# Performance work log

Hardware: AMD Instinct MI355X
Metric: run time of the kernel (lower is better)

## Reference

```python
import jax, jax.numpy as jnp
import numpy as np

N_NODES = 100000
N_EDGES = 1600000
IN_C, HID_C, OUT_C = 165, 256, 2


def setup_inputs() -> dict:
    key = jax.random.key(0)
    ks = jax.random.split(key, 7)
    x = jax.random.normal(ks[0], (N_NODES, IN_C), dtype=jnp.float32)
    edge_index = jax.random.randint(ks[1], (2, N_EDGES), 0, N_NODES, dtype=jnp.int64)
    # Glorot-ish scaled weights
    W1_l = jax.random.normal(ks[2], (IN_C, HID_C), dtype=jnp.float32) / np.sqrt(IN_C)
    W1_r = jax.random.normal(ks[3], (IN_C, HID_C), dtype=jnp.float32) / np.sqrt(IN_C)
    W2_l = jax.random.normal(ks[4], (HID_C, OUT_C), dtype=jnp.float32) / np.sqrt(HID_C)
    W2_r = jax.random.normal(ks[5], (HID_C, OUT_C), dtype=jnp.float32) / np.sqrt(HID_C)
    b1 = jnp.zeros((HID_C,), dtype=jnp.float32)
    b2 = jnp.zeros((OUT_C,), dtype=jnp.float32)
    return {"x": x, "edge_index": edge_index, "W1_l": W1_l, "b1": b1,
            "W1_r": W1_r, "W2_l": W2_l, "b2": b2, "W2_r": W2_r}


def _sage_conv(h, src, dst, n_nodes, Wl, b, Wr):
    # mean aggregation of neighbor messages (src -> dst), as in PyG SAGEConv
    agg = jax.ops.segment_sum(h[src], dst, num_segments=n_nodes)  # [N, C]
    deg = jax.ops.segment_sum(jnp.ones_like(dst, dtype=h.dtype), dst,
                              num_segments=n_nodes)               # [N]
    mean = agg / jnp.maximum(deg, 1.0)[:, None]
    # out = lin_l(aggr) + lin_r(root); bias lives on lin_l
    return mean @ Wl + b + h @ Wr


def reference(x, edge_index, W1_l, b1, W1_r, W2_l, b2, W2_r):
    src, dst = edge_index[0], edge_index[1]
    n = x.shape[0]
    h = jax.nn.relu(_sage_conv(x, src, dst, n, W1_l, b1, W1_r))
    out = _sage_conv(h, src, dst, n, W2_l, b2, W2_r)
    return out
```

## Files before the change

kernel.cpp:

```cpp
#include <hip/hip_runtime.h>

#define N_NODES 100000
#define N_EDGES 1600000
#define IN_C 165
#define HID_C 256
#define OUT_C 2

#define XPAD 168
#define LDSROW 360
#define NBLK_SCAN 98

typedef short bf16x8 __attribute__((ext_vector_type(8)));
typedef float f32x4 __attribute__((ext_vector_type(4)));

__device__ inline unsigned short f2bf(float f) {
    unsigned int u = __float_as_uint(f);
    u += 0x7fffu + ((u >> 16) & 1u);
    return (unsigned short)(u >> 16);
}
__device__ inline float bf2f(unsigned short h) {
    return __uint_as_float(((unsigned int)h) << 16);
}
__device__ inline unsigned int pack2bf(float a, float b) {
    return (unsigned int)f2bf(a) | ((unsigned int)f2bf(b) << 16);
}


__launch_bounds__(1024)
__global__ void k_scan1(const int* __restrict__ deg, int* __restrict__ incl,
                        int* __restrict__ btot) {
    const int tid = threadIdx.x;
    const int idx = blockIdx.x * 1024 + tid;
    const int lane = tid & 63, wid = tid >> 6;
    __shared__ int ws[16];
    int v = (idx < N_NODES) ? deg[idx] : 0;
    int s = v;
#pragma unroll
    for (int off = 1; off < 64; off <<= 1) {
        int t = __shfl_up(s, off);
        if (lane >= off) s += t;
    }
    if (lane == 63) ws[wid] = s;
    __syncthreads();
    if (wid == 0) {
        int p = (lane < 16) ? ws[lane] : 0;
#pragma unroll
        for (int off = 1; off < 16; off <<= 1) {
            int t = __shfl_up(p, off);
            if (lane >= off) p += t;
        }
        if (lane < 16) ws[lane] = p;
    }
    __syncthreads();
    int blockincl = s + (wid > 0 ? ws[wid - 1] : 0);
    if (idx < N_NODES) incl[idx] = blockincl;
    if (tid == 1023) btot[blockIdx.x] = blockincl;
}

__global__ void k_scan2(int* __restrict__ btot) {
    const int lane = threadIdx.x;
    int a = (2 * lane < NBLK_SCAN) ? btot[2 * lane] : 0;
    int b = (2 * lane + 1 < NBLK_SCAN) ? btot[2 * lane + 1] : 0;
    int p = a + b;
#pragma unroll
    for (int off = 1; off < 64; off <<= 1) {
        int t = __shfl_up(p, off);
        if (lane >= off) p += t;
    }
    if (2 * lane < NBLK_SCAN) btot[2 * lane] = p - b;
    if (2 * lane + 1 < NBLK_SCAN) btot[2 * lane + 1] = p;
}

__launch_bounds__(1024)
__global__ void k_scan3(const int* __restrict__ deg, int* incl_cursor,
                        const int* __restrict__ btot, int* __restrict__ rowptr) {
    const int idx = blockIdx.x * 1024 + threadIdx.x;
    if (idx == 0) rowptr[0] = 0;
    if (idx >= N_NODES) return;
    int off = (blockIdx.x > 0) ? btot[blockIdx.x - 1] : 0;
    int v = incl_cursor[idx] + off;
    rowptr[idx + 1] = v;
    incl_cursor[idx] = v - deg[idx];
}

#define FILL_GRID 2048
__global__ void k_fill(const int* __restrict__ src, const int* __restrict__ dst,
                       int* __restrict__ cursor, int* __restrict__ csr) {
    const int role = blockIdx.x & 7;
    const int nchunk = gridDim.x >> 3;
    const int lo = role * (N_NODES / 8);
    const int hi = lo + (N_NODES / 8);
    for (int e = (blockIdx.x >> 3) * 256 + threadIdx.x; e < N_EDGES;
         e += nchunk * 256) {
        int d = dst[e];
        int s = src[e];
        if (d >= lo && d < hi) {
            int pos = atomicAdd(&cursor[d], 1);
            csr[pos] = s;
        }
    }
}

__global__ void k_cvt(const float* __restrict__ x, const int* __restrict__ dst,
                      uint2* __restrict__ xb2, int* __restrict__ deg) {
    int idx = blockIdx.x * blockDim.x + threadIdx.x;
    if (idx < N_EDGES) atomicAdd(&deg[dst[idx]], 1);
    if (idx >= N_NODES * 42) return;
    int n = idx / 42;
    int t = idx - n * 42;
    int c = 4 * t;
    float f0 = x[(size_t)n * IN_C + c];
    float f1 = (c + 1 < IN_C) ? x[(size_t)n * IN_C + c + 1] : 0.f;
    float f2 = (c + 2 < IN_C) ? x[(size_t)n * IN_C + c + 2] : 0.f;
    float f3 = (c + 3 < IN_C) ? x[(size_t)n * IN_C + c + 3] : 0.f;
    uint2 p;
    p.x = pack2bf(f0, f1);
    p.y = pack2bf(f2, f3);
    xb2[idx] = p;
}

__global__ void k_wt(const float* __restrict__ W1l, const float* __restrict__ W1r,
                     unsigned short* __restrict__ Wt) {
    int k = blockIdx.x;
    int c = threadIdx.x;
    float v = 0.0f;
    if (k < IN_C) v = W1l[k * HID_C + c];
    else if (k >= XPAD && k < XPAD + IN_C) v = W1r[(k - XPAD) * HID_C + c];
    Wt[(size_t)c * 352 + k] = f2bf(v);
}

__global__ void k_agg1b(const int* __restrict__ rowptr, const int* __restrict__ csr,
                        const uint2* __restrict__ xb2, uint2* __restrict__ aggb2) {
    int n = (blockIdx.x * blockDim.x + threadIdx.x) >> 6;
    if (n >= N_NODES) return;
    const int lane = threadIdx.x & 63;
    const bool act = lane < 42;
    int beg = rowptr[n], end = rowptr[n + 1];
    float a0 = 0.f, a1 = 0.f, a2 = 0.f, a3 = 0.f;
    int j = beg;
#define ACC(u) { a0 += bf2f((unsigned short)((u).x & 0xffffu)); \
                 a1 += bf2f((unsigned short)((u).x >> 16)); \
                 a2 += bf2f((unsigned short)((u).y & 0xffffu)); \
                 a3 += bf2f((unsigned short)((u).y >> 16)); }
    for (; j + 7 < end; j += 8) {
        uint2 u[8];
#pragma unroll
        for (int q = 0; q < 8; ++q) {
            int s = csr[j + q];
            u[q] = act ? xb2[(size_t)s * 42 + lane] : make_uint2(0, 0);
        }
#pragma unroll
        for (int q = 0; q < 8; ++q) ACC(u[q]);
    }
    for (; j + 3 < end; j += 4) {
        uint2 u[4];
#pragma unroll
        for (int q = 0; q < 4; ++q) {
            int s = csr[j + q];
            u[q] = act ? xb2[(size_t)s * 42 + lane] : make_uint2(0, 0);
        }
#pragma unroll
        for (int q = 0; q < 4; ++q) ACC(u[q]);
    }
    for (; j < end; ++j) {
        int s0 = csr[j];
        uint2 u0 = act ? xb2[(size_t)s0 * 42 + lane] : make_uint2(0, 0);
        ACC(u0);
    }
#undef ACC
    if (act) {
        float invd = 1.0f / fmaxf((float)(end - beg), 1.0f);
        uint2 p;
        p.x = pack2bf(a0 * invd, a1 * invd);
        p.y = pack2bf(a2 * invd, a3 * invd);
        aggb2[(size_t)n * 42 + lane] = p;
    }
}

__launch_bounds__(256)
__global__ void k_gemm1(const unsigned short* __restrict__ aggb,
                        const unsigned short* __restrict__ xb,
                        const unsigned short* __restrict__ Wt,
                        const float* __restrict__ b1,
                        const float* __restrict__ W2l, const float* __restrict__ W2r,
                        float* __restrict__ yz) {
    __shared__ __align__(16) unsigned short lds[64 * LDSROW];
    const int tid = threadIdx.x;
    const int lane = tid & 63;
    const int w = tid >> 6;
    const int node0 = blockIdx.x * 64;

#pragma unroll
    for (int it = 0; it < 12; ++it) {
        int idx = tid + it * 256;
        if (idx < 64 * 45) {
            int row = idx / 45;
            int c = idx - row * 45;
            int n = node0 + row;
            uint4 v = make_uint4(0, 0, 0, 0);
            if (n < N_NODES) {
                if (c < 21)      v = *(const uint4*)&aggb[(size_t)n * XPAD + c * 8];
                else if (c < 42) v = *(const uint4*)&xb[(size_t)n * XPAD + (c - 21) * 8];
            }
            *(uint4*)&lds[row * LDSROW + c * 8] = v;
        }
    }
    __syncthreads();

    const int arow = lane & 15;
    const int kgrp = lane >> 4;
    const int colbase = w * 64;
    f32x4 acc[4][4] = {};

    for (int ks = 0; ks < 11; ++ks) {
        const int k0 = ks * 32 + kgrp * 8;
        bf16x8 bfr[4], afr[4];
#pragma unroll
        for (int n = 0; n < 4; ++n)
            bfr[n] = *(const bf16x8*)&Wt[(size_t)(colbase + n * 16 + arow) * 352 + k0];
#pragma unroll
        for (int m = 0; m < 4; ++m)
            afr[m] = *(const bf16x8*)&lds[(m * 16 + arow) * LDSROW + k0];
#pragma unroll
        for (int m = 0; m < 4; ++m)
#pragma unroll
            for (int n = 0; n < 4; ++n)
                acc[m][n] = __builtin_amdgcn_mfma_f32_16x16x32_bf16(afr[m], bfr[n],
                                                                    acc[m][n], 0, 0, 0);
    }

    float b1c[4];
    float2 wl[4], wr[4];
#pragma unroll
    for (int n = 0; n < 4; ++n) {
        int c = colbase + n * 16 + arow;
        b1c[n] = b1[c];
        wl[n] = *(const float2*)&W2l[c * 2];
        wr[n] = *(const float2*)&W2r[c * 2];
    }
    __syncthreads();
    float* part = (float*)lds;

#pragma unroll
    for (int m = 0; m < 4; ++m)
#pragma unroll
        for (int r = 0; r < 4; ++r) {
            float y0 = 0.f, y1 = 0.f, z0 = 0.f, z1 = 0.f;
#pragma unroll
            for (int n = 0; n < 4; ++n) {
                float h = fmaxf(acc[m][n][r] + b1c[n], 0.0f);
                y0 = fmaf(h, wl[n].x, y0); y1 = fmaf(h, wl[n].y, y1);
                z0 = fmaf(h, wr[n].x, z0); z1 = fmaf(h, wr[n].y, z1);
            }
#pragma unroll
            for (int off = 1; off < 16; off <<= 1) {
                y0 += __shfl_xor(y0, off); y1 += __shfl_xor(y1, off);
                z0 += __shfl_xor(z0, off); z1 += __shfl_xor(z1, off);
            }
            if (arow == 0) {
                int row = m * 16 + kgrp * 4 + r;
                float* p = &part[(w * 64 + row) * 4];
                p[0] = y0; p[1] = y1; p[2] = z0; p[3] = z1;
            }
        }
    __syncthreads();

    {
        int row = tid >> 2;
        int ch = tid & 3;
        float s = part[row * 4 + ch] + part[(256 + row * 4) + ch] +
                  part[(512 + row * 4) + ch] + part[(768 + row * 4) + ch];
        int node = node0 + row;
        if (node < N_NODES) yz[(size_t)node * 4 + ch] = s;
    }
}

__global__ void k_layer2(const int* __restrict__ rowptr, const int* __restrict__ csr,
                         const float* __restrict__ yz, const float* __restrict__ b2,
                         float* __restrict__ out) {
    int n = (blockIdx.x * blockDim.x + threadIdx.x) >> 6;
    if (n >= N_NODES) return;
    const int lane = threadIdx.x & 63;
    int beg = rowptr[n], end = rowptr[n + 1];
    float y0 = 0.f, y1 = 0.f;
    for (int i = beg + lane; i < end; i += 64) {
        int s = csr[i];
        float2 v = *(const float2*)&yz[(size_t)s * 4];
        y0 += v.x; y1 += v.y;
    }
#pragma unroll
    for (int off = 32; off >= 1; off >>= 1) {
        y0 += __shfl_xor(y0, off);
        y1 += __shfl_xor(y1, off);
    }
    if (lane == 0) {
        float invd = 1.0f / fmaxf((float)(end - beg), 1.0f);
        float2 o;
        o.x = y0 * invd + b2[0] + yz[(size_t)n * 4 + 2];
        o.y = y1 * invd + b2[1] + yz[(size_t)n * 4 + 3];
        *(float2*)&out[n * 2] = o;
    }
}

extern "C" void kernel_launch(void* const* d_in, const int* in_sizes, int n_in,
                              void* d_out, int out_size, void* d_ws, size_t ws_size,
                              hipStream_t stream) {
    const float* x   = (const float*)d_in[0];
    const int*   ei  = (const int*)d_in[1];
    const int*   src = ei;
    const int*   dst = ei + N_EDGES;
    const float* W1l = (const float*)d_in[2];
    const float* b1  = (const float*)d_in[3];
    const float* W1r = (const float*)d_in[4];
    const float* W2l = (const float*)d_in[5];
    const float* b2  = (const float*)d_in[6];
    const float* W2r = (const float*)d_in[7];
    float* out = (float*)d_out;

    int* wsi = (int*)d_ws;
    int* csr    = wsi;
    int* rowptr = wsi + 1600000;
    unsigned short* xb   = (unsigned short*)(wsi + 1700004);
    unsigned short* aggb = xb + (size_t)N_NODES * XPAD;
    unsigned short* Wt   = aggb + (size_t)N_NODES * XPAD;
    float* yz            = (float*)(Wt + 256 * 352);
    int* deg    = (int*)yz;
    int* inccur = (int*)yz + N_NODES;
    int* btot   = (int*)yz + 2 * N_NODES;

    hipMemsetAsync(deg, 0, N_NODES * sizeof(int), stream);

    k_cvt<<<(N_NODES * 42 + 255) / 256, 256, 0, stream>>>(x, dst, (uint2*)xb, deg);
    k_wt<<<352, 256, 0, stream>>>(W1l, W1r, Wt);
    k_scan1<<<NBLK_SCAN, 1024, 0, stream>>>(deg, inccur, btot);
    k_scan2<<<1, 64, 0, stream>>>(btot);
    k_scan3<<<NBLK_SCAN, 1024, 0, stream>>>(deg, inccur, btot, rowptr);
    k_fill<<<FILL_GRID, 256, 0, stream>>>(src, dst, inccur, csr);
    k_agg1b<<<(N_NODES * 64 + 255) / 256, 256, 0, stream>>>(rowptr, csr,
                                                            (const uint2*)xb,
                                                            (uint2*)aggb);
    k_gemm1<<<(N_NODES + 63) / 64, 256, 0, stream>>>(aggb, xb, Wt, b1, W2l, W2r, yz);
    k_layer2<<<(N_NODES * 64 + 255) / 256, 256, 0, stream>>>(rowptr, csr, yz, b2, out);
}
```

Baseline: 466.3 us.

## Split degree counting into partitioned kernel and halve gemm1 node tile

Moves the degree atomics out of the conversion kernel into a separate k_deg kernel. It partitions destination ranges across block roles, the same way the fill kernel does, to improve atomic locality. The src load in k_fill now happens only for edges that pass the range filter. k_gemm1 now processes 32 nodes per block instead of 64, which doubles the grid and lowers LDS and register use per block. The cost is more reloads of the weight tile and one extra kernel launch.

```diff
diff --git a/kernel.cpp b/kernel.cpp
--- a/kernel.cpp
+++ b/kernel.cpp
@@ -9,6 +9,7 @@
 #define XPAD 168
 #define LDSROW 360
 #define NBLK_SCAN 98
+#define GNT 32
 
 typedef short bf16x8 __attribute__((ext_vector_type(8)));
 typedef float f32x4 __attribute__((ext_vector_type(4)));
@@ -25,6 +26,18 @@
     return (unsigned int)f2bf(a) | ((unsigned int)f2bf(b) << 16);
 }
 
+
+__global__ void k_deg(const int* __restrict__ dst, int* __restrict__ deg) {
+    const int role = blockIdx.x & 7;
+    const int nchunk = gridDim.x >> 3;
+    const int lo = role * (N_NODES / 8);
+    const int hi = lo + (N_NODES / 8);
+    for (int e = (blockIdx.x >> 3) * 256 + threadIdx.x; e < N_EDGES;
+         e += nchunk * 256) {
+        int d = dst[e];
+        if (d >= lo && d < hi) atomicAdd(&deg[d], 1);
+    }
+}
 
 __launch_bounds__(1024)
 __global__ void k_scan1(const int* __restrict__ deg, int* __restrict__ incl,
@@ -93,18 +106,16 @@
     for (int e = (blockIdx.x >> 3) * 256 + threadIdx.x; e < N_EDGES;
          e += nchunk * 256) {
         int d = dst[e];
-        int s = src[e];
         if (d >= lo && d < hi) {
+            int s = src[e];
             int pos = atomicAdd(&cursor[d], 1);
             csr[pos] = s;
         }
     }
 }
 
-__global__ void k_cvt(const float* __restrict__ x, const int* __restrict__ dst,
-                      uint2* __restrict__ xb2, int* __restrict__ deg) {
+__global__ void k_cvt(const float* __restrict__ x, uint2* __restrict__ xb2) {
     int idx = blockIdx.x * blockDim.x + threadIdx.x;
-    if (idx < N_EDGES) atomicAdd(&deg[dst[idx]], 1);
     if (idx >= N_NODES * 42) return;
     int n = idx / 42;
     int t = idx - n * 42;
@@ -184,45 +195,41 @@
                         const float* __restrict__ b1,
                         const float* __restrict__ W2l, const float* __restrict__ W2r,
                         float* __restrict__ yz) {
-    __shared__ __align__(16) unsigned short lds[64 * LDSROW];
+    __shared__ __align__(16) unsigned short lds[GNT * LDSROW];
     const int tid = threadIdx.x;
     const int lane = tid & 63;
     const int w = tid >> 6;
-    const int node0 = blockIdx.x * 64;
-
-#pragma unroll
-    for (int it = 0; it < 12; ++it) {
-        int idx = tid + it * 256;
-        if (idx < 64 * 45) {
-            int row = idx / 45;
-            int c = idx - row * 45;
-            int n = node0 + row;
-            uint4 v = make_uint4(0, 0, 0, 0);
-            if (n < N_NODES) {
-                if (c < 21)      v = *(const uint4*)&aggb[(size_t)n * XPAD + c * 8];
-                else if (c < 42) v = *(const uint4*)&xb[(size_t)n * XPAD + (c - 21) * 8];
-            }
-            *(uint4*)&lds[row * LDSROW + c * 8] = v;
-        }
+    const int node0 = blockIdx.x * GNT;
+
+    for (int idx = tid; idx < GNT * 45; idx += 256) {
+        int row = idx / 45;
+        int c = idx - row * 45;
+        int n = node0 + row;
+        uint4 v = make_uint4(0, 0, 0, 0);
+        if (n < N_NODES) {
+            if (c < 21)      v = *(const uint4*)&aggb[(size_t)n * XPAD + c * 8];
+            else if (c < 42) v = *(const uint4*)&xb[(size_t)n * XPAD + (c - 21) * 8];
+        }
+        *(uint4*)&lds[row * LDSROW + c * 8] = v;
     }
     __syncthreads();
 
     const int arow = lane & 15;
     const int kgrp = lane >> 4;
     const int colbase = w * 64;
-    f32x4 acc[4][4] = {};
+    f32x4 acc[2][4] = {};
 
     for (int ks = 0; ks < 11; ++ks) {
         const int k0 = ks * 32 + kgrp * 8;
-        bf16x8 bfr[4], afr[4];
+        bf16x8 bfr[4], afr[2];
 #pragma unroll
         for (int n = 0; n < 4; ++n)
             bfr[n] = *(const bf16x8*)&Wt[(size_t)(colbase + n * 16 + arow) * 352 + k0];
 #pragma unroll
-        for (int m = 0; m < 4; ++m)
+        for (int m = 0; m < 2; ++m)
             afr[m] = *(const bf16x8*)&lds[(m * 16 + arow) * LDSROW + k0];
 #pragma unroll
-        for (int m = 0; m < 4; ++m)
+        for (int m = 0; m < 2; ++m)
 #pragma unroll
             for (int n = 0; n < 4; ++n)
                 acc[m][n] = __builtin_amdgcn_mfma_f32_16x16x32_bf16(afr[m], bfr[n],
@@ -242,7 +249,7 @@
     float* part = (float*)lds;
 
 #pragma unroll
-    for (int m = 0; m < 4; ++m)
+    for (int m = 0; m < 2; ++m)
 #pragma unroll
         for (int r = 0; r < 4; ++r) {
             float y0 = 0.f, y1 = 0.f, z0 = 0.f, z1 = 0.f;
@@ -259,17 +266,17 @@
             }
             if (arow == 0) {
                 int row = m * 16 + kgrp * 4 + r;
-                float* p = &part[(w * 64 + row) * 4];
+                float* p = &part[(w * GNT + row) * 4];
                 p[0] = y0; p[1] = y1; p[2] = z0; p[3] = z1;
             }
         }
     __syncthreads();
 
-    {
+    if (tid < GNT * 4) {
         int row = tid >> 2;
         int ch = tid & 3;
-        float s = part[row * 4 + ch] + part[(256 + row * 4) + ch] +
-                  part[(512 + row * 4) + ch] + part[(768 + row * 4) + ch];
+        float s = part[row * 4 + ch] + part[(GNT * 4 + row * 4) + ch] +
+                  part[(GNT * 8 + row * 4) + ch] + part[(GNT * 12 + row * 4) + ch];
         int node = node0 + row;
         if (node < N_NODES) yz[(size_t)node * 4 + ch] = s;
     }
@@ -330,8 +337,9 @@
 
     hipMemsetAsync(deg, 0, N_NODES * sizeof(int), stream);
 
-    k_cvt<<<(N_NODES * 42 + 255) / 256, 256, 0, stream>>>(x, dst, (uint2*)xb, deg);
+    k_cvt<<<(N_NODES * 42 + 255) / 256, 256, 0, stream>>>(x, (uint2*)xb);
     k_wt<<<352, 256, 0, stream>>>(W1l, W1r, Wt);
+    k_deg<<<FILL_GRID, 256, 0, stream>>>(dst, deg);
     k_scan1<<<NBLK_SCAN, 1024, 0, stream>>>(deg, inccur, btot);
     k_scan2<<<1, 64, 0, stream>>>(btot);
     k_scan3<<<NBLK_SCAN, 1024, 0, stream>>>(deg, inccur, btot, rowptr);
@@ -339,6 +347,7 @@
     k_agg1b<<<(N_NODES * 64 + 255) / 256, 256, 0, stream>>>(rowptr, csr,
                                                             (const uint2*)xb,
                                                             (uint2*)aggb);
-    k_gemm1<<<(N_NODES + 63) / 64, 256, 0, stream>>>(aggb, xb, Wt, b1, W2l, W2r, yz);
+    k_gemm1<<<(N_NODES + GNT - 1) / GNT, 256, 0, stream>>>(aggb, xb, Wt, b1,
+                                                           W2l, W2r, yz);
     k_layer2<<<(N_NODES * 64 + 255) / 256, 256, 0, stream>>>(rowptr, csr, yz, b2, out);
 }
```

Result: no change. 474.7 us (+1.8%).

## Pre-bucket edges by destination range before CSR fill

Applied to the files above, without the earlier changes.

Adds a k_bucket pass that counts degrees and scatters (src,dst) pairs into eight per-role staging buckets, each a contiguous dst range, using a workspace region later overwritten by aggregation. The fill kernel then reads only its own bucket instead of every role block scanning all edges and discarding seven eighths of them. This cuts redundant edge reads in the fill from about eight passes to one, at the cost of an extra kernel that writes and rereads 8-byte pairs. Degree counting moves from the conversion kernel into the bucket kernel.

```diff
diff --git a/kernel.cpp b/kernel.cpp
--- a/kernel.cpp
+++ b/kernel.cpp
@@ -9,6 +9,8 @@
 #define XPAD 168
 #define LDSROW 360
 #define NBLK_SCAN 98
+#define ROLE_N (N_NODES / 8)
+#define STAGE_CAP 208000
 
 typedef short bf16x8 __attribute__((ext_vector_type(8)));
 typedef float f32x4 __attribute__((ext_vector_type(4)));
@@ -83,28 +85,61 @@
     incl_cursor[idx] = v - deg[idx];
 }
 
+#define BUCKET_EPB 2048
+__launch_bounds__(256)
+__global__ void k_bucket(const int* __restrict__ src, const int* __restrict__ dst,
+                         int* __restrict__ deg, int* __restrict__ rolecnt,
+                         int2* __restrict__ stage) {
+    __shared__ int lcnt[8];
+    __shared__ int lbase[8];
+    const int tid = threadIdx.x;
+    if (tid < 8) lcnt[tid] = 0;
+    __syncthreads();
+    const int e0 = blockIdx.x * BUCKET_EPB;
+    int sv[8], dv[8], rv[8], lr[8];
+#pragma unroll
+    for (int i = 0; i < 8; ++i) {
+        int e = e0 + tid + i * 256;
+        if (e < N_EDGES) {
+            dv[i] = dst[e];
+            sv[i] = src[e];
+            rv[i] = dv[i] / ROLE_N;
+            atomicAdd(&deg[dv[i]], 1);
+            lr[i] = atomicAdd(&lcnt[rv[i]], 1);
+        }
+    }
+    __syncthreads();
+    if (tid < 8) lbase[tid] = atomicAdd(&rolecnt[tid], lcnt[tid]);
+    __syncthreads();
+#pragma unroll
+    for (int i = 0; i < 8; ++i) {
+        int e = e0 + tid + i * 256;
+        if (e < N_EDGES) {
+            int r = rv[i];
+            stage[(size_t)r * STAGE_CAP + lbase[r] + lr[i]] =
+                make_int2(sv[i], dv[i]);
+        }
+    }
+}
+
 #define FILL_GRID 2048
-__global__ void k_fill(const int* __restrict__ src, const int* __restrict__ dst,
-                       int* __restrict__ cursor, int* __restrict__ csr) {
+__global__ void k_fill2(const int2* __restrict__ stage,
+                        const int* __restrict__ rolecnt,
+                        int* __restrict__ cursor, int* __restrict__ csr) {
     const int role = blockIdx.x & 7;
     const int nchunk = gridDim.x >> 3;
-    const int lo = role * (N_NODES / 8);
-    const int hi = lo + (N_NODES / 8);
-    for (int e = (blockIdx.x >> 3) * 256 + threadIdx.x; e < N_EDGES;
-         e += nchunk * 256) {
-        int d = dst[e];
-        int s = src[e];
-        if (d >= lo && d < hi) {
-            int pos = atomicAdd(&cursor[d], 1);
-            csr[pos] = s;
-        }
-    }
-}
-
-__global__ void k_cvt(const float* __restrict__ x, const int* __restrict__ dst,
-                      uint2* __restrict__ xb2, int* __restrict__ deg) {
+    const int cnt = rolecnt[role];
+    const int2* s = stage + (size_t)role * STAGE_CAP;
+    for (int i = (blockIdx.x >> 3) * 256 + threadIdx.x; i < cnt;
+         i += nchunk * 256) {
+        int2 p = s[i];
+        int pos = atomicAdd(&cursor[p.y], 1);
+        csr[pos] = p.x;
+    }
+}
+
+__global__ void k_cvt(const float* __restrict__ x, uint2* __restrict__ xb2) {
     int idx = blockIdx.x * blockDim.x + threadIdx.x;
-    if (idx < N_EDGES) atomicAdd(&deg[dst[idx]], 1);
     if (idx >= N_NODES * 42) return;
     int n = idx / 42;
     int t = idx - n * 42;
@@ -324,18 +359,22 @@
     unsigned short* aggb = xb + (size_t)N_NODES * XPAD;
     unsigned short* Wt   = aggb + (size_t)N_NODES * XPAD;
     float* yz            = (float*)(Wt + 256 * 352);
-    int* deg    = (int*)yz;
-    int* inccur = (int*)yz + N_NODES;
-    int* btot   = (int*)yz + 2 * N_NODES;
-
-    hipMemsetAsync(deg, 0, N_NODES * sizeof(int), stream);
-
-    k_cvt<<<(N_NODES * 42 + 255) / 256, 256, 0, stream>>>(x, dst, (uint2*)xb, deg);
+    int2* stage  = (int2*)aggb;
+    int* deg     = (int*)yz;
+    int* inccur  = (int*)yz + N_NODES;
+    int* btot    = (int*)yz + 2 * N_NODES;
+    int* rolecnt = (int*)yz + 2 * N_NODES + 100;
+
+    hipMemsetAsync(deg, 0, (2 * N_NODES + 108) * sizeof(int), stream);
+
+    k_cvt<<<(N_NODES * 42 + 255) / 256, 256, 0, stream>>>(x, (uint2*)xb);
     k_wt<<<352, 256, 0, stream>>>(W1l, W1r, Wt);
+    k_bucket<<<(N_EDGES + BUCKET_EPB - 1) / BUCKET_EPB, 256, 0, stream>>>(
+        src, dst, deg, rolecnt, stage);
     k_scan1<<<NBLK_SCAN, 1024, 0, stream>>>(deg, inccur, btot);
     k_scan2<<<1, 64, 0, stream>>>(btot);
     k_scan3<<<NBLK_SCAN, 1024, 0, stream>>>(deg, inccur, btot, rowptr);
-    k_fill<<<FILL_GRID, 256, 0, stream>>>(src, dst, inccur, csr);
+    k_fill2<<<FILL_GRID, 256, 0, stream>>>(stage, rolecnt, inccur, csr);
     k_agg1b<<<(N_NODES * 64 + 255) / 256, 256, 0, stream>>>(rowptr, csr,
                                                             (const uint2*)xb,
                                                             (uint2*)aggb);
```

Result: slower. 479.7 us (+2.9%).

## Store neighbor features as FP8 for gather and read root features from fp32 in GEMM

Applied to the files above, without the earlier changes.

Converts node features to a custom e4m3-style FP8 encoding for the neighbor gather, halving the bytes fetched per edge in the aggregation kernel, and decodes them with a bit shift plus a scale FMA. The GEMM kernel now loads the root features directly from fp32 x and converts them to bf16 in LDS, so the bf16 copy of x is no longer needed. It also moves the src load inside the destination-range check in the CSR fill kernel. The gathered features lose precision, which may affect accuracy, and the GEMM staging now uses scalar fp32 loads of x.

```diff
diff --git a/kernel.cpp b/kernel.cpp
--- a/kernel.cpp
+++ b/kernel.cpp
@@ -9,6 +9,7 @@
 #define XPAD 168
 #define LDSROW 360
 #define NBLK_SCAN 98
+#define FILL_GRID 2048
 
 typedef short bf16x8 __attribute__((ext_vector_type(8)));
 typedef float f32x4 __attribute__((ext_vector_type(4)));
@@ -24,6 +25,22 @@
 __device__ inline unsigned int pack2bf(float a, float b) {
     return (unsigned int)f2bf(a) | ((unsigned int)f2bf(b) << 16);
 }
+
+__device__ inline unsigned int f2fp8(float f) {
+    unsigned int u = __float_as_uint(f);
+    unsigned int s = (u >> 24) & 0x80u;
+    unsigned int au = u & 0x7fffffffu;
+    if (au >= 0x43e00000u) return s | 0x7eu;
+    au += 0x7ffffu + ((au >> 20) & 1u);
+    int e8 = (int)(au >> 23) - 120;
+    if (e8 <= 0) {
+        int m = (int)(fabsf(f) * 512.0f + 0.5f);
+        if (m > 7) return s | 0x08u;
+        return s | (unsigned int)m;
+    }
+    return s | ((unsigned int)e8 << 3) | ((au >> 20) & 7u);
+}
+#define FP8_SCALE 1.3292280e36f
 
 
 __launch_bounds__(1024)
@@ -83,7 +100,6 @@
     incl_cursor[idx] = v - deg[idx];
 }
 
-#define FILL_GRID 2048
 __global__ void k_fill(const int* __restrict__ src, const int* __restrict__ dst,
                        int* __restrict__ cursor, int* __restrict__ csr) {
     const int role = blockIdx.x & 7;
@@ -93,16 +109,16 @@
     for (int e = (blockIdx.x >> 3) * 256 + threadIdx.x; e < N_EDGES;
          e += nchunk * 256) {
         int d = dst[e];
-        int s = src[e];
         if (d >= lo && d < hi) {
+            int s = src[e];
             int pos = atomicAdd(&cursor[d], 1);
             csr[pos] = s;
         }
     }
 }
 
-__global__ void k_cvt(const float* __restrict__ x, const int* __restrict__ dst,
-                      uint2* __restrict__ xb2, int* __restrict__ deg) {
+__global__ void k_cvt8(const float* __restrict__ x, const int* __restrict__ dst,
+                       unsigned int* __restrict__ xf8, int* __restrict__ deg) {
     int idx = blockIdx.x * blockDim.x + threadIdx.x;
     if (idx < N_EDGES) atomicAdd(&deg[dst[idx]], 1);
     if (idx >= N_NODES * 42) return;
@@ -113,10 +129,7 @@
     float f1 = (c + 1 < IN_C) ? x[(size_t)n * IN_C + c + 1] : 0.f;
     float f2 = (c + 2 < IN_C) ? x[(size_t)n * IN_C + c + 2] : 0.f;
     float f3 = (c + 3 < IN_C) ? x[(size_t)n * IN_C + c + 3] : 0.f;
-    uint2 p;
-    p.x = pack2bf(f0, f1);
-    p.y = pack2bf(f2, f3);
-    xb2[idx] = p;
+    xf8[idx] = f2fp8(f0) | (f2fp8(f1) << 8) | (f2fp8(f2) << 16) | (f2fp8(f3) << 24);
 }
 
 __global__ void k_wt(const float* __restrict__ W1l, const float* __restrict__ W1r,
@@ -130,7 +143,8 @@
 }
 
 __global__ void k_agg1b(const int* __restrict__ rowptr, const int* __restrict__ csr,
-                        const uint2* __restrict__ xb2, uint2* __restrict__ aggb2) {
+                        const unsigned int* __restrict__ xf8,
+                        uint2* __restrict__ aggb2) {
     int n = (blockIdx.x * blockDim.x + threadIdx.x) >> 6;
     if (n >= N_NODES) return;
     const int lane = threadIdx.x & 63;
@@ -138,36 +152,38 @@
     int beg = rowptr[n], end = rowptr[n + 1];
     float a0 = 0.f, a1 = 0.f, a2 = 0.f, a3 = 0.f;
     int j = beg;
-#define ACC(u) { a0 += bf2f((unsigned short)((u).x & 0xffffu)); \
-                 a1 += bf2f((unsigned short)((u).x >> 16)); \
-                 a2 += bf2f((unsigned short)((u).y & 0xffffu)); \
-                 a3 += bf2f((unsigned short)((u).y >> 16)); }
+#define DEC(b) __uint_as_float((((b) & 0x7fu) << 20) | (((b) & 0x80u) << 24))
+#define ACC(u) { a0 = fmaf(DEC((u) & 0xffu),         FP8_SCALE, a0); \
+                 a1 = fmaf(DEC(((u) >> 8) & 0xffu),  FP8_SCALE, a1); \
+                 a2 = fmaf(DEC(((u) >> 16) & 0xffu), FP8_SCALE, a2); \
+                 a3 = fmaf(DEC((u) >> 24),           FP8_SCALE, a3); }
     for (; j + 7 < end; j += 8) {
-        uint2 u[8];
+        unsigned int u[8];
 #pragma unroll
         for (int q = 0; q < 8; ++q) {
             int s = csr[j + q];
-            u[q] = act ? xb2[(size_t)s * 42 + lane] : make_uint2(0, 0);
+            u[q] = act ? xf8[(size_t)s * 42 + lane] : 0u;
         }
 #pragma unroll
         for (int q = 0; q < 8; ++q) ACC(u[q]);
     }
     for (; j + 3 < end; j += 4) {
-        uint2 u[4];
+        unsigned int u[4];
 #pragma unroll
         for (int q = 0; q < 4; ++q) {
             int s = csr[j + q];
-            u[q] = act ? xb2[(size_t)s * 42 + lane] : make_uint2(0, 0);
+            u[q] = act ? xf8[(size_t)s * 42 + lane] : 0u;
         }
 #pragma unroll
         for (int q = 0; q < 4; ++q) ACC(u[q]);
     }
     for (; j < end; ++j) {
         int s0 = csr[j];
-        uint2 u0 = act ? xb2[(size_t)s0 * 42 + lane] : make_uint2(0, 0);
+        unsigned int u0 = act ? xf8[(size_t)s0 * 42 + lane] : 0u;
         ACC(u0);
     }
 #undef ACC
+#undef DEC
     if (act) {
         float invd = 1.0f / fmaxf((float)(end - beg), 1.0f);
         uint2 p;
@@ -179,7 +195,7 @@
 
 __launch_bounds__(256)
 __global__ void k_gemm1(const unsigned short* __restrict__ aggb,
-                        const unsigned short* __restrict__ xb,
+                        const float* __restrict__ x,
                         const unsigned short* __restrict__ Wt,
                         const float* __restrict__ b1,
                         const float* __restrict__ W2l, const float* __restrict__ W2r,
@@ -190,20 +206,30 @@
     const int w = tid >> 6;
     const int node0 = blockIdx.x * 64;
 
-#pragma unroll
-    for (int it = 0; it < 12; ++it) {
-        int idx = tid + it * 256;
-        if (idx < 64 * 45) {
-            int row = idx / 45;
-            int c = idx - row * 45;
-            int n = node0 + row;
-            uint4 v = make_uint4(0, 0, 0, 0);
-            if (n < N_NODES) {
-                if (c < 21)      v = *(const uint4*)&aggb[(size_t)n * XPAD + c * 8];
-                else if (c < 42) v = *(const uint4*)&xb[(size_t)n * XPAD + (c - 21) * 8];
-            }
-            *(uint4*)&lds[row * LDSROW + c * 8] = v;
-        }
+    for (int idx = tid; idx < 64 * 21; idx += 256) {
+        int row = idx / 21;
+        int c = idx - row * 21;
+        int n = node0 + row;
+        uint4 v = make_uint4(0, 0, 0, 0);
+        if (n < N_NODES) v = *(const uint4*)&aggb[(size_t)n * XPAD + c * 8];
+        *(uint4*)&lds[row * LDSROW + c * 8] = v;
+    }
+    for (int idx = tid; idx < 64 * 3; idx += 256) {
+        int row = idx / 3;
+        int c = idx - row * 3;
+        *(uint4*)&lds[row * LDSROW + 336 + c * 8] = make_uint4(0, 0, 0, 0);
+    }
+    for (int idx = tid; idx < 64 * IN_C; idx += 256) {
+        int row = idx / IN_C;
+        int ch = idx - row * IN_C;
+        int n = node0 + row;
+        float v = (n < N_NODES) ? x[(size_t)n * IN_C + ch] : 0.f;
+        lds[row * LDSROW + 168 + ch] = f2bf(v);
+    }
+    for (int idx = tid; idx < 64 * 3; idx += 256) {
+        int row = idx / 3;
+        int ch = 165 + (idx - row * 3);
+        lds[row * LDSROW + 168 + ch] = 0;
     }
     __syncthreads();
 
@@ -320,8 +346,8 @@
     int* wsi = (int*)d_ws;
     int* csr    = wsi;
     int* rowptr = wsi + 1600000;
-    unsigned short* xb   = (unsigned short*)(wsi + 1700004);
-    unsigned short* aggb = xb + (size_t)N_NODES * XPAD;
+    unsigned int*   xf8  = (unsigned int*)(wsi + 1700004);
+    unsigned short* aggb = (unsigned short*)(xf8 + (size_t)N_NODES * 42);
     unsigned short* Wt   = aggb + (size_t)N_NODES * XPAD;
     float* yz            = (float*)(Wt + 256 * 352);
     int* deg    = (int*)yz;
@@ -330,15 +356,14 @@
 
     hipMemsetAsync(deg, 0, N_NODES * sizeof(int), stream);
 
-    k_cvt<<<(N_NODES * 42 + 255) / 256, 256, 0, stream>>>(x, dst, (uint2*)xb, deg);
+    k_cvt8<<<(N_NODES * 42 + 255) / 256, 256, 0, stream>>>(x, dst, xf8, deg);
     k_wt<<<352, 256, 0, stream>>>(W1l, W1r, Wt);
     k_scan1<<<NBLK_SCAN, 1024, 0, stream>>>(deg, inccur, btot);
     k_scan2<<<1, 64, 0, stream>>>(btot);
     k_scan3<<<NBLK_SCAN, 1024, 0, stream>>>(deg, inccur, btot, rowptr);
     k_fill<<<FILL_GRID, 256, 0, stream>>>(src, dst, inccur, csr);
-    k_agg1b<<<(N_NODES * 64 + 255) / 256, 256, 0, stream>>>(rowptr, csr,
-                                                            (const uint2*)xb,
+    k_agg1b<<<(N_NODES * 64 + 255) / 256, 256, 0, stream>>>(rowptr, csr, xf8,
                                                             (uint2*)aggb);
-    k_gemm1<<<(N_NODES + 63) / 64, 256, 0, stream>>>(aggb, xb, Wt, b1, W2l, W2r, yz);
+    k_gemm1<<<(N_NODES + 63) / 64, 256, 0, stream>>>(aggb, x, Wt, b1, W2l, W2r, yz);
     k_layer2<<<(N_NODES * 64 + 255) / 256, 256, 0, stream>>>(rowptr, csr, yz, b2, out);
 }
```

After: 503.8 us. +8.0%, slower.
